# Performance work log

Measured on AMD Instinct MI355X. Metric: run time of the kernel, lower is better.

## Reference

```python
import jax, jax.numpy as jnp
import numpy as np

NH = 1024
NV = 31
LAYERS = 2
BS = 64
SEQ = 512
EPS = 1e-5


def _gru_layer(x_seq, h0, Wih, Whh, bih, bhh):
    """x_seq: [B,S,in], h0: [B,nh]. PyTorch GRU gate math. Returns [B,S,nh], h_last."""
    # Precompute input-side gates for all timesteps: [B,S,3nh]
    xg = jnp.einsum('bsi,gi->bsg', x_seq, Wih) + bih
    xg = jnp.swapaxes(xg, 0, 1)  # [S,B,3nh] for scan over time

    def step(h, xg_t):
        hg = h @ Whh.T + bhh  # [B,3nh]
        xr, xz, xn = jnp.split(xg_t, 3, axis=-1)
        hr, hz, hn = jnp.split(hg, 3, axis=-1)
        r = jax.nn.sigmoid(xr + hr)
        z = jax.nn.sigmoid(xz + hz)
        n = jnp.tanh(xn + r * hn)
        h_new = (1.0 - z) * n + z * h
        return h_new, h_new

    h_last, ys = jax.lax.scan(step, h0, xg)
    return jnp.swapaxes(ys, 0, 1), h_last  # [B,S,nh]


def setup_inputs() -> dict:
    key = jax.random.key(0)
    ks = jax.random.split(key, 16)
    s = 0.02
    inp = {
        'x': jax.random.randint(ks[0], (BS, SEQ), 0, NV),
        'h0': jnp.zeros((LAYERS, BS, NH), jnp.float32),
        'emb': jax.random.normal(ks[1], (NV, NH), jnp.float32) * s,
        'Wih0': jax.random.normal(ks[2], (3 * NH, NH), jnp.float32) * s,
        'Whh0': jax.random.normal(ks[3], (3 * NH, NH), jnp.float32) * s,
        'bih0': jnp.zeros((3 * NH,), jnp.float32),
        'bhh0': jnp.zeros((3 * NH,), jnp.float32),
        'Wih1': jax.random.normal(ks[4], (3 * NH, NH), jnp.float32) * s,
        'Whh1': jax.random.normal(ks[5], (3 * NH, NH), jnp.float32) * s,
        'bih1': jnp.zeros((3 * NH,), jnp.float32),
        'bhh1': jnp.zeros((3 * NH,), jnp.float32),
        'gamma': jnp.ones((NH,), jnp.float32),
        'beta': jnp.zeros((NH,), jnp.float32),
        'Wout': jax.random.normal(ks[6], (NV, NH), jnp.float32) * s,
        'bout': jnp.zeros((NV,), jnp.float32),
    }
    return inp


def reference(x, h0, emb, Wih0, Whh0, bih0, bhh0, Wih1, Whh1, bih1, bhh1,
              gamma, beta, Wout, bout):
    e = emb[x]  # [B,S,nh] embedding lookup
    y0, _ = _gru_layer(e, h0[0], Wih0, Whh0, bih0, bhh0)
    y1, _ = _gru_layer(y0, h0[1], Wih1, Whh1, bih1, bhh1)
    # BatchNorm1dFlat: flatten (B*S, nh), batch-statistics BN, reshape back
    flat = y1.reshape(-1, NH)
    mu = flat.mean(axis=0)
    var = flat.var(axis=0)  # biased, as in BN training
    bn = (y1 - mu) * jax.lax.rsqrt(var + EPS) * gamma + beta
    return bn @ Wout.T + bout  # [B,S,nv]
```

## Files before the change

kernel.cpp:

```cpp
#include <hip/hip_runtime.h>
#include <cstddef>
#include <stdint.h>

#define NHID 1024
#define NVOC 31
#define NB   64
#define NSEQ 512
#define NWRK 192
#define NGRID 256
#define NTHR 512
#define EPSV 1e-5f
#define RS   68
#define RS2  36
#define SL   (NB*NHID)
#define XG_SLOTS 16

typedef __attribute__((ext_vector_type(8))) short short8;
typedef __attribute__((ext_vector_type(4))) float float4v;

#define OFF_F0  0
#define OFF_F1  4096
#define OFF_F2  8192
#define OFF_FIN 12288
#define CNT_BYTES 12352

#define M_OFF_Y0  12544
#define M_OFF_Y1  (M_OFF_Y0 + 513ull*SL*2)
#define M_OFF_H1I (M_OFF_Y1 + 512ull*SL*2)
#define M_OFF_T0  (M_OFF_H1I + (unsigned long long)SL*2)
#define M_OFF_ST  (M_OFF_T0 + 31ull*3*NHID*4)
#define M_OFF_XG  (M_OFF_ST + 16384ull)

#define LDS_BYTES 65024

__device__ __forceinline__ unsigned short f2bf(float f){
  unsigned u = __builtin_bit_cast(unsigned, f);
  u += 0x7fffu + ((u >> 16) & 1u);
  return (unsigned short)(u >> 16);
}
__device__ __forceinline__ float bf2f(unsigned short h){
  unsigned u = ((unsigned)h) << 16;
  return __builtin_bit_cast(float, u);
}
__device__ __forceinline__ float sigm(float x){ return 1.f/(1.f + __expf(-x)); }
__device__ __forceinline__ float tanh_f(float x){ return 1.f - 2.f/(__expf(2.f*x) + 1.f); }

__device__ __forceinline__ void burn(float& d){
#pragma unroll
  for (int i=0;i<16;++i)
    asm volatile("v_fmac_f32 %0, %1, %2" : "+v"(d) : "v"(d), "v"(d));
}

__device__ __forceinline__ void setflag(unsigned* f, unsigned v){
  __hip_atomic_store(f, v, __ATOMIC_RELAXED, __HIP_MEMORY_SCOPE_AGENT);
}
__device__ __forceinline__ void waitflags64(const unsigned* f, int target, int lane, float& d){
  const unsigned* p = f + (size_t)lane*16;
  for(;;){
    int v = (int)__hip_atomic_load(p, __ATOMIC_RELAXED, __HIP_MEMORY_SCOPE_AGENT);
    if (__all(v >= target)) break;
    burn(d);
  }
  asm volatile("" ::: "memory");
}
__device__ __forceinline__ void waitflags32(const unsigned* f, int base32, int target, int lane, float& d){
  const unsigned* p = f + (size_t)(base32 + (lane & 31))*16;
  for(;;){
    int v = (int)__hip_atomic_load(p, __ATOMIC_RELAXED, __HIP_MEMORY_SCOPE_AGENT);
    if (__all(v >= target)) break;
    burn(d);
  }
  asm volatile("" ::: "memory");
}
__device__ __forceinline__ void waitflags2(const unsigned* f, int base2, int target, int lane, float& d){
  const unsigned* p = f + (size_t)(base2 + (lane & 1))*16;
  for(;;){
    int v = (int)__hip_atomic_load(p, __ATOMIC_RELAXED, __HIP_MEMORY_SCOPE_AGENT);
    if (__all(v >= target)) break;
    burn(d);
  }
  asm volatile("" ::: "memory");
}
__device__ __forceinline__ void waitflags_slow64(const unsigned* f, int target, int lane, float& d){
  const unsigned* p = f + (size_t)lane*16;
  for(;;){
    int v = (int)__hip_atomic_load(p, __ATOMIC_RELAXED, __HIP_MEMORY_SCOPE_AGENT);
    if (__all(v >= target)) break;
    burn(d); burn(d); burn(d); burn(d);
  }
  asm volatile("" ::: "memory");
}
__device__ __forceinline__ void sig(unsigned* c){
  __hip_atomic_fetch_add(c, 1u, __ATOMIC_RELAXED, __HIP_MEMORY_SCOPE_AGENT);
}
__device__ __forceinline__ void waitc(unsigned* c, unsigned v, float& d){
  while (__hip_atomic_load(c, __ATOMIC_RELAXED, __HIP_MEMORY_SCOPE_AGENT) < v)
    burn(d);
}

__device__ __forceinline__ void stc16(void* p, short8 v){
  asm volatile("global_store_dwordx4 %0, %1, off sc1"
               :: "v"((unsigned long long)(uintptr_t)p), "v"(v) : "memory");
}
__device__ __forceinline__ void stc4(void* p, float v){
  asm volatile("global_store_dword %0, %1, off sc1"
               :: "v"((unsigned long long)(uintptr_t)p), "v"(v) : "memory");
}
__device__ __forceinline__ void drain_vm(){
  asm volatile("s_waitcnt vmcnt(0)" ::: "memory");
}

__device__ __forceinline__ void load_a16_plain(const unsigned short* base, short8 (&f)[4][4]){
#pragma unroll
  for (int r=0;r<4;++r){
    const short8* p = (const short8*)(base + (size_t)r*16*NHID);
#pragma unroll
    for (int kt=0;kt<4;++kt) f[r][kt] = p[kt*4];
  }
}
__device__ __forceinline__ void gemm_frags(const short8 (&f)[4][4],
                                           const short8 (&bfr)[3][4],
                                           float* red, int lane, int wid)
{
  const int l15 = lane & 15, q = lane >> 4;
  float4v acc[4][3];
#pragma unroll
  for (int mt=0; mt<4; ++mt)
#pragma unroll
    for (int nt=0; nt<3; ++nt) acc[mt][nt] = (float4v){0.f,0.f,0.f,0.f};
#pragma unroll
  for (int kt=0; kt<4; ++kt){
#pragma unroll
    for (int nt=0; nt<3; ++nt){
      acc[0][nt] = __builtin_amdgcn_mfma_f32_16x16x32_bf16(f[0][kt], bfr[nt][kt], acc[0][nt],0,0,0);
      acc[1][nt] = __builtin_amdgcn_mfma_f32_16x16x32_bf16(f[1][kt], bfr[nt][kt], acc[1][nt],0,0,0);
      acc[2][nt] = __builtin_amdgcn_mfma_f32_16x16x32_bf16(f[2][kt], bfr[nt][kt], acc[2][nt],0,0,0);
      acc[3][nt] = __builtin_amdgcn_mfma_f32_16x16x32_bf16(f[3][kt], bfr[nt][kt], acc[3][nt],0,0,0);
    }
  }
  if (wid >= 4){
#pragma unroll
    for (int mt=0; mt<4; ++mt)
#pragma unroll
      for (int nt=0; nt<3; ++nt){
        int n = nt*16 + l15, row = mt*16 + q*4;
        *(float4v*)(red + ((wid-4)*48 + n)*RS + row) = acc[mt][nt];
      }
  }
  __syncthreads();
  if (wid < 4){
#pragma unroll
    for (int mt=0; mt<4; ++mt)
#pragma unroll
      for (int nt=0; nt<3; ++nt){
        int n = nt*16 + l15, row = mt*16 + q*4;
        float4v* p = (float4v*)(red + (wid*48 + n)*RS + row);
        float4v v = *p;
        *p = v + acc[mt][nt];
      }
  }
  __syncthreads();
}
__device__ __forceinline__ void load_bfrags(const float* W, const int* rowbase,
                                            short8 (&bfr)[3][4], int lane, int wid)
{
  const int l15 = lane & 15, q = lane >> 4;
#pragma unroll
  for (int nt=0; nt<3; ++nt){
    const float* wp0 = W + (size_t)(rowbase[nt] + l15)*NHID + wid*128 + q*8;
#pragma unroll
    for (int kt=0; kt<4; ++kt){
      const float* wp = wp0 + kt*32;
      short8 fr;
#pragma unroll
      for (int j=0;j<8;++j) fr[j] = (short)f2bf(wp[j]);
      bfr[nt][kt] = fr;
    }
  }
}

__device__ __forceinline__ void load_bfrags6(const float* W, int ch0,
                                             short8 (&bfr)[6][4], int lane, int wid)
{
  const int l15 = lane & 15, q = lane >> 4;
#pragma unroll
  for (int nt=0; nt<6; ++nt){
    int grow = (nt>>1)*NHID + ch0 + (nt&1)*16 + l15;
    const float* wp0 = W + (size_t)grow*NHID + wid*128 + q*8;
#pragma unroll
    for (int kt=0; kt<4; ++kt){
      const float* wp = wp0 + kt*32;
      short8 fr;
#pragma unroll
      for (int j=0;j<8;++j) fr[j] = (short)f2bf(wp[j]);
      bfr[nt][kt] = fr;
    }
  }
}
__device__ __forceinline__ void load_a2(const unsigned short* slab, int b0,
                                        short8 (&f)[2][4], int lane, int wid)
{
#pragma unroll
  for (int mt=0;mt<2;++mt){
    const short8* p = (const short8*)(slab + (size_t)(b0 + mt*16 + (lane&15))*NHID
                                      + wid*128 + (lane>>4)*8);
#pragma unroll
    for (int kt=0;kt<4;++kt) f[mt][kt] = p[kt*4];
  }
}
__device__ __forceinline__ void gemm2d(const short8 (&fA)[2][4],
                                       const short8 (&bfr)[6][4],
                                       float* red, int lane, int wid)
{
  const int l15 = lane & 15, q = lane >> 4;
  float4v acc[2][6];
#pragma unroll
  for (int mt=0; mt<2; ++mt)
#pragma unroll
    for (int nt=0; nt<6; ++nt) acc[mt][nt] = (float4v){0.f,0.f,0.f,0.f};
#pragma unroll
  for (int kt=0; kt<4; ++kt){
#pragma unroll
    for (int nt=0; nt<6; ++nt){
      acc[0][nt] = __builtin_amdgcn_mfma_f32_16x16x32_bf16(fA[0][kt], bfr[nt][kt], acc[0][nt],0,0,0);
      acc[1][nt] = __builtin_amdgcn_mfma_f32_16x16x32_bf16(fA[1][kt], bfr[nt][kt], acc[1][nt],0,0,0);
    }
  }
  if (wid >= 4){
#pragma unroll
    for (int mt=0; mt<2; ++mt)
#pragma unroll
      for (int nt=0; nt<6; ++nt){
        int n = nt*16 + l15, row = mt*16 + q*4;
        *(float4v*)(red + ((wid-4)*96 + n)*RS2 + row) = acc[mt][nt];
      }
  }
  __syncthreads();
  if (wid < 4){
#pragma unroll
    for (int mt=0; mt<2; ++mt)
#pragma unroll
      for (int nt=0; nt<6; ++nt){
        int n = nt*16 + l15, row = mt*16 + q*4;
        float4v* p = (float4v*)(red + (wid*96 + n)*RS2 + row);
        float4v v = *p;
        *p = v + acc[mt][nt];
      }
  }
  __syncthreads();
}

__global__ __launch_bounds__(NTHR, 2) void mgru_fused(
    const int*   __restrict__ x,    const float* __restrict__ h0,
    const float* __restrict__ emb,
    const float* __restrict__ Wih0, const float* __restrict__ Whh0,
    const float* __restrict__ bih0, const float* __restrict__ bhh0,
    const float* __restrict__ Wih1, const float* __restrict__ Whh1,
    const float* __restrict__ bih1, const float* __restrict__ bhh1,
    const float* __restrict__ gamma, const float* __restrict__ beta,
    const float* __restrict__ Wout, const float* __restrict__ bout,
    float* __restrict__ out, char* ws)
{
  __shared__ __align__(16) char smem[LDS_BYTES];
  float* red = (float*)smem;

  unsigned* f0  = (unsigned*)(ws + OFF_F0);
  unsigned* f1  = (unsigned*)(ws + OFF_F1);
  unsigned* f2  = (unsigned*)(ws + OFF_F2);
  unsigned* fin = (unsigned*)(ws + OFF_FIN);
  unsigned short* y0b   = (unsigned short*)(ws + M_OFF_Y0);
  unsigned short* y1    = (unsigned short*)(ws + M_OFF_Y1);
  unsigned short* h1i   = (unsigned short*)(ws + M_OFF_H1I);
  float*          T0    = (float*)(ws + M_OFF_T0);
  float*          stats = (float*)(ws + M_OFF_ST);
  float*          xgring= (float*)(ws + M_OFF_XG);

  const int tid  = threadIdx.x;
  const int lane = tid & 63;
  const int wid  = tid >> 6;
  const int wg   = blockIdx.x;
  const int l15 = lane & 15, q = lane >> 4;
  float dummy = (float)tid * 1e-30f + 1.0f;

  if (wg >= NWRK){
    for(;;){
      for (int i=0;i<64;++i) burn(dummy);
      unsigned v = __hip_atomic_load(fin, __ATOMIC_RELAXED, __HIP_MEMORY_SCOPE_AGENT);
      if (v >= (unsigned)NWRK) break;
    }
    if (tid == 0) __threadfence();
    __syncthreads();
    if (dummy == 1234.5678f) ((volatile float*)smem)[0] = dummy;
    goto epilogue;
  }

  {
    if (tid == 0) __threadfence();
    __syncthreads();

    const int role = (wg < 64) ? 0 : (wg < 128 ? 1 : 2);

    if (role == 0){
      const int rw = wg, bg = rw >> 5, cg = rw & 31;
      const int b0 = bg*32, ch0 = cg*32;
      const int fidx = bg*32 + cg;
      const int g = tid;
      const int b = b0 + (g & 31);
      const int oct = g >> 5;
      short8 bfr0[6][4];
      float hprev[8] = {0,0,0,0,0,0,0,0};
      float br[8], bz[8], bn[8];

      if (tid < 128){
        short8 pk;
#pragma unroll
        for (int j=0;j<8;++j){
          int ch = ch0 + oct*8 + j;
          hprev[j] = h0[(size_t)b*NHID + ch];
          br[j] = bhh0[ch]; bz[j] = bhh0[NHID + ch]; bn[j] = bhh0[2*NHID + ch];
          pk[j] = (short)f2bf(hprev[j]);
        }
        stc16(y0b + (size_t)b*NHID + ch0 + oct*8, pk);
        drain_vm();
      }
      __syncthreads();
      if (tid == 0) setflag(f0 + (size_t)fidx*16, 1u);

      for (int e = tid; e < NVOC*96; e += NTHR){
        int v = e / 96, n = e - v*96;
        int gate = n >> 5, c32 = n & 31;
        int grow = gate*NHID + ch0 + c32;
        const float4v* e4 = (const float4v*)(emb  + (size_t)v*NHID);
        const float4v* w4 = (const float4v*)(Wih0 + (size_t)grow*NHID);
        float acc = 0.f;
        for (int k=0;k<NHID/4;++k){
          float4v a = e4[k], bb = w4[k];
          acc += a[0]*bb[0] + a[1]*bb[1] + a[2]*bb[2] + a[3]*bb[3];
        }
        T0[(size_t)v*3*NHID + grow] = acc + bih0[grow];
      }
      load_bfrags6(Whh0, ch0, bfr0, lane, wid);
      __syncthreads();

      for (int t = 0; t < NSEQ; ++t){
        waitflags32(f0, bg*32, t+1, lane, dummy);
        short8 fA[2][4];
        load_a2(y0b + (size_t)t*SL, b0, fA, lane, wid);
        gemm2d(fA, bfr0, red, lane, wid);
        if (tid < 128){
          int tok = x[(size_t)b*NSEQ + t];
          const float* tp = T0 + (size_t)tok*3*NHID;
          int m = g & 31;
          short8 pk;
#pragma unroll
          for (int j=0;j<8;++j){
            int c32 = oct*8 + j, ch = ch0 + c32;
            float hr = br[j], hz = bz[j], hn = bn[j];
#pragma unroll
            for (int w=0;w<4;++w){
              hr += red[(w*96 +      c32)*RS2 + m];
              hz += red[(w*96 + 32 + c32)*RS2 + m];
              hn += red[(w*96 + 64 + c32)*RS2 + m];
            }
            float r = sigm(tp[ch] + hr);
            float z = sigm(tp[NHID + ch] + hz);
            float n = tanh_f(tp[2*NHID + ch] + r*hn);
            float hnv = (1.f - z)*n + z*hprev[j];
            hprev[j] = hnv;
            pk[j] = (short)f2bf(hnv);
          }
          stc16(y0b + (size_t)(t+1)*SL + (size_t)b*NHID + ch0 + oct*8, pk);
          drain_vm();
        }
        __syncthreads();
        if (tid == 0) setflag(f0 + (size_t)fidx*16, (unsigned)(t+2));
      }

    } else if (role == 1){
      const int sub = wg - 64, ch0 = sub*16;
      int rowbase[3] = {ch0, NHID + ch0, 2*NHID + ch0};
      short8 wf[3][4];
      load_bfrags(Wih1, rowbase, wf, lane, wid);
      __syncthreads();

      for (int t = 0; t < NSEQ; ++t){
        if ((t & 3) == 0 && t >= 16)
          waitflags_slow64(f2, t-11, lane, dummy);
        waitflags64(f0, t+2, lane, dummy);
        short8 fB[4][4];
        load_a16_plain(y0b + (size_t)(t+1)*SL + (size_t)l15*NHID + wid*128 + q*8, fB);
        gemm_frags(fB, wf, red, lane, wid);
        float* xgw = xgring + ((size_t)(t & (XG_SLOTS-1))*64 + (size_t)sub)*3072;
#pragma unroll
        for (int i=0;i<6;++i){
          int idx = tid + i*512;
          int n = idx >> 6, row = idx & 63;
          float v = bih1[(n>>4)*NHID + ch0 + (n&15)];
          v += red[(      n)*RS + row];
          v += red[( 48 + n)*RS + row];
          v += red[( 96 + n)*RS + row];
          v += red[(144 + n)*RS + row];
          stc4(xgw + idx, v);
        }
        drain_vm();
        __syncthreads();
        if (tid == 0) setflag(f1 + (size_t)sub*16, (unsigned)(t+2));
      }

    } else {
      const int rw = wg - 128, bg = rw >> 5, cg = rw & 31;
      const int b0 = bg*32, ch0 = cg*32;
      const int fidx = bg*32 + cg;
      const int g = tid;
      const int b = b0 + (g & 31);
      const int oct = g >> 5;
      short8 bfrH[6][4];
      float hprev[8] = {0,0,0,0,0,0,0,0};
      float bhr[8], bhz[8], bhn[8];
      float s1[8] = {0,0,0,0,0,0,0,0}, s2[8] = {0,0,0,0,0,0,0,0};

      if (tid < 128){
        short8 pk;
#pragma unroll
        for (int j=0;j<8;++j){
          int ch = ch0 + oct*8 + j;
          hprev[j] = h0[(size_t)NB*NHID + (size_t)b*NHID + ch];
          bhr[j] = bhh1[ch]; bhz[j] = bhh1[NHID + ch]; bhn[j] = bhh1[2*NHID + ch];
          pk[j] = (short)f2bf(hprev[j]);
        }
        stc16(h1i + (size_t)b*NHID + ch0 + oct*8, pk);
        drain_vm();
      }
      __syncthreads();
      if (tid == 0) setflag(f2 + (size_t)fidx*16, 1u);

      load_bfrags6(Whh1, ch0, bfrH, lane, wid);
      __syncthreads();

      for (int t = 0; t < NSEQ; ++t){
        waitflags32(f2, bg*32, t+1, lane, dummy);
        const unsigned short* hsrc = (t == 0) ? h1i : (y1 + (size_t)(t-1)*SL);
        short8 fH[2][4];
        load_a2(hsrc, b0, fH, lane, wid);
        gemm2d(fH, bfrH, red, lane, wid);
        float hrv[8], hzv[8], hnv_[8];
        if (tid < 128){
          int m = g & 31;
#pragma unroll
          for (int j=0;j<8;++j){
            int c32 = oct*8 + j;
            float hr = bhr[j], hz = bhz[j], hn = bhn[j];
#pragma unroll
            for (int w=0;w<4;++w){
              hr += red[(w*96 +      c32)*RS2 + m];
              hz += red[(w*96 + 32 + c32)*RS2 + m];
              hn += red[(w*96 + 64 + c32)*RS2 + m];
            }
            hrv[j] = hr; hzv[j] = hz; hnv_[j] = hn;
          }
        }
        waitflags2(f1, cg*2, t+2, lane, dummy);
        if (tid < 128){
          const float* xgp = xgring + (size_t)(t & (XG_SLOTS-1))*64*3072;
          short8 pk;
#pragma unroll
          for (int j=0;j<8;++j){
            int ch = ch0 + oct*8 + j;
            int sub1 = ch >> 4, c16 = ch & 15;
            const float* q0 = xgp + (size_t)sub1*3072 + (size_t)c16*64 + b;
            float xr = __hip_atomic_load(q0,           __ATOMIC_RELAXED, __HIP_MEMORY_SCOPE_AGENT);
            float xz = __hip_atomic_load(q0 + 16*64,   __ATOMIC_RELAXED, __HIP_MEMORY_SCOPE_AGENT);
            float xn = __hip_atomic_load(q0 + 32*64,   __ATOMIC_RELAXED, __HIP_MEMORY_SCOPE_AGENT);
            float r  = sigm(xr + hrv[j]);
            float z  = sigm(xz + hzv[j]);
            float nn = tanh_f(xn + r*hnv_[j]);
            float hnew = (1.f - z)*nn + z*hprev[j];
            hprev[j] = hnew;
            unsigned short hb = f2bf(hnew);
            pk[j] = (short)hb;
            float hq = bf2f(hb);
            s1[j] += hq; s2[j] += hq*hq;
          }
          stc16(y1 + (size_t)t*SL + (size_t)b*NHID + ch0 + oct*8, pk);
          drain_vm();
        }
        __syncthreads();
        if (tid == 0) setflag(f2 + (size_t)fidx*16, (unsigned)(t+2));
      }

      {
        float* sb = (float*)smem;
        __syncthreads();
        if (tid < 128){
#pragma unroll
          for (int j=0;j<8;++j) sb[(oct*8 + j)*32 + (g & 31)] = s1[j];
        }
        __syncthreads();
        if (tid < 32){
          float a = 0.f;
          for (int i=0;i<32;++i) a += sb[tid*32 + i];
          stats[(size_t)bg*2048 + ch0 + tid] = a;
        }
        __syncthreads();
        if (tid < 128){
#pragma unroll
          for (int j=0;j<8;++j) sb[(oct*8 + j)*32 + (g & 31)] = s2[j];
        }
        __syncthreads();
        if (tid < 32){
          float a = 0.f;
          for (int i=0;i<32;++i) a += sb[tid*32 + i];
          stats[(size_t)bg*2048 + 1024 + ch0 + tid] = a;
        }
      }
    }

    __syncthreads();
    if (tid == 0){
      __threadfence();
      sig(fin);
      waitc(fin, NWRK, dummy);
      __threadfence();
    }
    __syncthreads();
    if (dummy == 1234.5678f) ((volatile float*)smem)[0] = dummy;
  }

epilogue:
  {
    const float inv_n = 1.f/32768.f;

    float* bpart    = (float*)smem;
    float* bprime_l = (float*)(smem + 2048);
    {
      int v = tid >> 4, k0 = tid & 15;
      float partial = 0.f;
      if (v < NVOC){
        for (int k = k0; k < NHID; k += 16){
          float s1k = stats[k] + stats[2048 + k];
          float s2k = stats[1024 + k] + stats[3072 + k];
          float mu  = s1k*inv_n;
          float var = s2k*inv_n - mu*mu;
          float sc  = gamma[k]*rsqrtf(var + EPSV);
          partial += (beta[k] - mu*sc) * Wout[(size_t)v*NHID + k];
        }
      }
      bpart[tid] = partial;
    }
    __syncthreads();
    if (tid < 32){
      float bpv = 0.f;
      for (int j=0;j<16;++j) bpv += bpart[tid*16 + j];
      bprime_l[tid] = (tid < NVOC) ? (bpv + bout[tid]) : 0.f;
    }
    __syncthreads();
    float bp_a = bprime_l[l15];
    float bp_b = (l15 < 15) ? bprime_l[16 + l15] : 0.f;
    __syncthreads();

    unsigned short* wsc = (unsigned short*)smem;
    for (int e = tid; e < NVOC*1032; e += NTHR){
      int v = e / 1032, k = e - v*1032;
      float val = 0.f;
      if (k < NHID){
        float s1k = stats[k] + stats[2048 + k];
        float s2k = stats[1024 + k] + stats[3072 + k];
        float mu  = s1k*inv_n;
        float var = s2k*inv_n - mu*mu;
        float sc  = gamma[k]*rsqrtf(var + EPSV);
        val = Wout[(size_t)v*NHID + k] * sc;
      }
      wsc[e] = f2bf(val);
    }
    __syncthreads();

    int wglob = wg*8 + wid;
    if ((wglob & 3) == 0){
      int J = wglob >> 2;
      float4v acc[4][2];
#pragma unroll
      for (int mt=0;mt<4;++mt){ acc[mt][0] = (float4v){0,0,0,0}; acc[mt][1] = (float4v){0,0,0,0}; }
      const unsigned short* abase = y1 + (size_t)(J*64 + l15)*NHID + q*8;
      const short8 zero8 = (short8){0,0,0,0,0,0,0,0};
#pragma unroll 4
      for (int kt=0; kt<32; ++kt){
        short8 bv0 = *(const short8*)(wsc + (size_t)l15*1032 + kt*32 + q*8);
        short8 bv1 = (l15 < 15) ? *(const short8*)(wsc + (size_t)(16+l15)*1032 + kt*32 + q*8) : zero8;
        short8 a0 = *(const short8*)(abase + (size_t)kt*32);
        short8 a1 = *(const short8*)(abase + 16*NHID + (size_t)kt*32);
        short8 a2 = *(const short8*)(abase + 32*NHID + (size_t)kt*32);
        short8 a3 = *(const short8*)(abase + 48*NHID + (size_t)kt*32);
        acc[0][0] = __builtin_amdgcn_mfma_f32_16x16x32_bf16(a0, bv0, acc[0][0],0,0,0);
        acc[1][0] = __builtin_amdgcn_mfma_f32_16x16x32_bf16(a1, bv0, acc[1][0],0,0,0);
        acc[2][0] = __builtin_amdgcn_mfma_f32_16x16x32_bf16(a2, bv0, acc[2][0],0,0,0);
        acc[3][0] = __builtin_amdgcn_mfma_f32_16x16x32_bf16(a3, bv0, acc[3][0],0,0,0);
        acc[0][1] = __builtin_amdgcn_mfma_f32_16x16x32_bf16(a0, bv1, acc[0][1],0,0,0);
        acc[1][1] = __builtin_amdgcn_mfma_f32_16x16x32_bf16(a1, bv1, acc[1][1],0,0,0);
        acc[2][1] = __builtin_amdgcn_mfma_f32_16x16x32_bf16(a2, bv1, acc[2][1],0,0,0);
        acc[3][1] = __builtin_amdgcn_mfma_f32_16x16x32_bf16(a3, bv1, acc[3][1],0,0,0);
      }
#pragma unroll
      for (int mt=0;mt<4;++mt){
#pragma unroll
        for (int nt=0;nt<2;++nt){
          int v = nt*16 + l15;
          if (v < NVOC){
            float bpv = (nt==0) ? bp_a : bp_b;
            int r0 = J*64 + mt*16 + q*4;
#pragma unroll
            for (int i2=0;i2<4;++i2){
              int r = r0 + i2;
              int bb = r & 63, tt = r >> 6;
              out[(size_t)(bb*NSEQ + tt)*NVOC + v] = acc[mt][nt][i2] + bpv;
            }
          }
        }
      }
    }
  }
}

extern "C" void kernel_launch(void* const* d_in, const int* in_sizes, int n_in,
                              void* d_out, int out_size, void* d_ws, size_t ws_size,
                              hipStream_t stream) {
  (void)in_sizes; (void)n_in; (void)out_size; (void)ws_size;
  hipMemsetAsync(d_ws, 0, CNT_BYTES, stream);
  mgru_fused<<<dim3(NGRID), dim3(NTHR), 0, stream>>>(
      (const int*)d_in[0],  (const float*)d_in[1],  (const float*)d_in[2],
      (const float*)d_in[3], (const float*)d_in[4], (const float*)d_in[5],
      (const float*)d_in[6], (const float*)d_in[7], (const float*)d_in[8],
      (const float*)d_in[9], (const float*)d_in[10], (const float*)d_in[11],
      (const float*)d_in[12], (const float*)d_in[13], (const float*)d_in[14],
      (float*)d_out, (char*)d_ws);
}
```

Baseline: 4.171 ms.

## Retile layer-1 input-gate workers into 32-batch by 32-channel blocks with per-block flags

Layer-1 input-projection workgroups previously each covered 16 channels across all 64 batch rows and waited on all 64 layer-0 flags. They now each own a 32-batch by 32-channel tile, reuse the 2D GEMM helpers, and wait only on the 32 layer-0 flags of their batch group. Each consumer waits on a single matching producer flag and reads a contiguous xg tile. This narrows cross-workgroup dependencies so layer 1 can begin as soon as its batch half is ready. The cost is more weight fragments held in registers per workgroup.

```diff
diff --git a/kernel.cpp b/kernel.cpp
--- a/kernel.cpp
+++ b/kernel.cpp
@@ -10,7 +10,6 @@
 #define NGRID 256
 #define NTHR 512
 #define EPSV 1e-5f
-#define RS   68
 #define RS2  36
 #define SL   (NB*NHID)
 #define XG_SLOTS 16
@@ -54,15 +53,6 @@
 __device__ __forceinline__ void setflag(unsigned* f, unsigned v){
   __hip_atomic_store(f, v, __ATOMIC_RELAXED, __HIP_MEMORY_SCOPE_AGENT);
 }
-__device__ __forceinline__ void waitflags64(const unsigned* f, int target, int lane, float& d){
-  const unsigned* p = f + (size_t)lane*16;
-  for(;;){
-    int v = (int)__hip_atomic_load(p, __ATOMIC_RELAXED, __HIP_MEMORY_SCOPE_AGENT);
-    if (__all(v >= target)) break;
-    burn(d);
-  }
-  asm volatile("" ::: "memory");
-}
 __device__ __forceinline__ void waitflags32(const unsigned* f, int base32, int target, int lane, float& d){
   const unsigned* p = f + (size_t)(base32 + (lane & 31))*16;
   for(;;){
@@ -72,20 +62,15 @@
   }
   asm volatile("" ::: "memory");
 }
-__device__ __forceinline__ void waitflags2(const unsigned* f, int base2, int target, int lane, float& d){
-  const unsigned* p = f + (size_t)(base2 + (lane & 1))*16;
-  for(;;){
-    int v = (int)__hip_atomic_load(p, __ATOMIC_RELAXED, __HIP_MEMORY_SCOPE_AGENT);
-    if (__all(v >= target)) break;
+__device__ __forceinline__ void waitflag1(const unsigned* f, int idx, int target, float& d){
+  const unsigned* p = f + (size_t)idx*16;
+  while ((int)__hip_atomic_load(p, __ATOMIC_RELAXED, __HIP_MEMORY_SCOPE_AGENT) < target)
     burn(d);
-  }
   asm volatile("" ::: "memory");
 }
-__device__ __forceinline__ void waitflags_slow64(const unsigned* f, int target, int lane, float& d){
-  const unsigned* p = f + (size_t)lane*16;
-  for(;;){
-    int v = (int)__hip_atomic_load(p, __ATOMIC_RELAXED, __HIP_MEMORY_SCOPE_AGENT);
-    if (__all(v >= target)) break;
+__device__ __forceinline__ void waitflag1_slow(const unsigned* f, int idx, int target, float& d){
+  const unsigned* p = f + (size_t)idx*16;
+  while ((int)__hip_atomic_load(p, __ATOMIC_RELAXED, __HIP_MEMORY_SCOPE_AGENT) < target){
     burn(d); burn(d); burn(d); burn(d);
   }
   asm volatile("" ::: "memory");
@@ -108,75 +93,6 @@
 }
 __device__ __forceinline__ void drain_vm(){
   asm volatile("s_waitcnt vmcnt(0)" ::: "memory");
-}
-
-__device__ __forceinline__ void load_a16_plain(const unsigned short* base, short8 (&f)[4][4]){
-#pragma unroll
-  for (int r=0;r<4;++r){
-    const short8* p = (const short8*)(base + (size_t)r*16*NHID);
-#pragma unroll
-    for (int kt=0;kt<4;++kt) f[r][kt] = p[kt*4];
-  }
-}
-__device__ __forceinline__ void gemm_frags(const short8 (&f)[4][4],
-                                           const short8 (&bfr)[3][4],
-                                           float* red, int lane, int wid)
-{
-  const int l15 = lane & 15, q = lane >> 4;
-  float4v acc[4][3];
-#pragma unroll
-  for (int mt=0; mt<4; ++mt)
-#pragma unroll
-    for (int nt=0; nt<3; ++nt) acc[mt][nt] = (float4v){0.f,0.f,0.f,0.f};
-#pragma unroll
-  for (int kt=0; kt<4; ++kt){
-#pragma unroll
-    for (int nt=0; nt<3; ++nt){
-      acc[0][nt] = __builtin_amdgcn_mfma_f32_16x16x32_bf16(f[0][kt], bfr[nt][kt], acc[0][nt],0,0,0);
-      acc[1][nt] = __builtin_amdgcn_mfma_f32_16x16x32_bf16(f[1][kt], bfr[nt][kt], acc[1][nt],0,0,0);
-      acc[2][nt] = __builtin_amdgcn_mfma_f32_16x16x32_bf16(f[2][kt], bfr[nt][kt], acc[2][nt],0,0,0);
-      acc[3][nt] = __builtin_amdgcn_mfma_f32_16x16x32_bf16(f[3][kt], bfr[nt][kt], acc[3][nt],0,0,0);
-    }
-  }
-  if (wid >= 4){
-#pragma unroll
-    for (int mt=0; mt<4; ++mt)
-#pragma unroll
-      for (int nt=0; nt<3; ++nt){
-        int n = nt*16 + l15, row = mt*16 + q*4;
-        *(float4v*)(red + ((wid-4)*48 + n)*RS + row) = acc[mt][nt];
-      }
-  }
-  __syncthreads();
-  if (wid < 4){
-#pragma unroll
-    for (int mt=0; mt<4; ++mt)
-#pragma unroll
-      for (int nt=0; nt<3; ++nt){
-        int n = nt*16 + l15, row = mt*16 + q*4;
-        float4v* p = (float4v*)(red + (wid*48 + n)*RS + row);
-        float4v v = *p;
-        *p = v + acc[mt][nt];
-      }
-  }
-  __syncthreads();
-}
-__device__ __forceinline__ void load_bfrags(const float* W, const int* rowbase,
-                                            short8 (&bfr)[3][4], int lane, int wid)
-{
-  const int l15 = lane & 15, q = lane >> 4;
-#pragma unroll
-  for (int nt=0; nt<3; ++nt){
-    const float* wp0 = W + (size_t)(rowbase[nt] + l15)*NHID + wid*128 + q*8;
-#pragma unroll
-    for (int kt=0; kt<4; ++kt){
-      const float* wp = wp0 + kt*32;
-      short8 fr;
-#pragma unroll
-      for (int j=0;j<8;++j) fr[j] = (short)f2bf(wp[j]);
-      bfr[nt][kt] = fr;
-    }
-  }
 }
 
 __device__ __forceinline__ void load_bfrags6(const float* W, int ch0,
@@ -377,34 +293,35 @@
       }
 
     } else if (role == 1){
-      const int sub = wg - 64, ch0 = sub*16;
-      int rowbase[3] = {ch0, NHID + ch0, 2*NHID + ch0};
-      short8 wf[3][4];
-      load_bfrags(Wih1, rowbase, wf, lane, wid);
+      const int rw = wg - 64, bg = rw >> 5, cg = rw & 31;
+      const int b0 = bg*32, ch0 = cg*32;
+      const int fidx = bg*32 + cg;
+      short8 wf[6][4];
+      load_bfrags6(Wih1, ch0, wf, lane, wid);
       __syncthreads();
 
       for (int t = 0; t < NSEQ; ++t){
         if ((t & 3) == 0 && t >= 16)
-          waitflags_slow64(f2, t-11, lane, dummy);
-        waitflags64(f0, t+2, lane, dummy);
-        short8 fB[4][4];
-        load_a16_plain(y0b + (size_t)(t+1)*SL + (size_t)l15*NHID + wid*128 + q*8, fB);
-        gemm_frags(fB, wf, red, lane, wid);
-        float* xgw = xgring + ((size_t)(t & (XG_SLOTS-1))*64 + (size_t)sub)*3072;
+          waitflag1_slow(f2, fidx, t-11, dummy);
+        waitflags32(f0, bg*32, t+2, lane, dummy);
+        short8 fB[2][4];
+        load_a2(y0b + (size_t)(t+1)*SL, b0, fB, lane, wid);
+        gemm2d(fB, wf, red, lane, wid);
+        float* xgw = xgring + ((size_t)(t & (XG_SLOTS-1))*64 + (size_t)fidx)*3072;
 #pragma unroll
         for (int i=0;i<6;++i){
           int idx = tid + i*512;
-          int n = idx >> 6, row = idx & 63;
-          float v = bih1[(n>>4)*NHID + ch0 + (n&15)];
-          v += red[(      n)*RS + row];
-          v += red[( 48 + n)*RS + row];
-          v += red[( 96 + n)*RS + row];
-          v += red[(144 + n)*RS + row];
+          int n = idx >> 5, m = idx & 31;
+          float v = bih1[(n>>5)*NHID + ch0 + (n&31)];
+          v += red[(      n)*RS2 + m];
+          v += red[( 96 + n)*RS2 + m];
+          v += red[(192 + n)*RS2 + m];
+          v += red[(288 + n)*RS2 + m];
           stc4(xgw + idx, v);
         }
         drain_vm();
         __syncthreads();
-        if (tid == 0) setflag(f1 + (size_t)sub*16, (unsigned)(t+2));
+        if (tid == 0) setflag(f1 + (size_t)fidx*16, (unsigned)(t+2));
       }
 
     } else {
@@ -459,18 +376,17 @@
             hrv[j] = hr; hzv[j] = hz; hnv_[j] = hn;
           }
         }
-        waitflags2(f1, cg*2, t+2, lane, dummy);
+        waitflag1(f1, fidx, t+2, dummy);
         if (tid < 128){
-          const float* xgp = xgring + (size_t)(t & (XG_SLOTS-1))*64*3072;
+          const float* xgt = xgring + ((size_t)(t & (XG_SLOTS-1))*64 + (size_t)fidx)*3072;
+          int m = g & 31;
           short8 pk;
 #pragma unroll
           for (int j=0;j<8;++j){
-            int ch = ch0 + oct*8 + j;
-            int sub1 = ch >> 4, c16 = ch & 15;
-            const float* q0 = xgp + (size_t)sub1*3072 + (size_t)c16*64 + b;
-            float xr = __hip_atomic_load(q0,           __ATOMIC_RELAXED, __HIP_MEMORY_SCOPE_AGENT);
-            float xz = __hip_atomic_load(q0 + 16*64,   __ATOMIC_RELAXED, __HIP_MEMORY_SCOPE_AGENT);
-            float xn = __hip_atomic_load(q0 + 32*64,   __ATOMIC_RELAXED, __HIP_MEMORY_SCOPE_AGENT);
+            int c32 = oct*8 + j;
+            float xr = __hip_atomic_load(xgt + (size_t)(     c32)*32 + m, __ATOMIC_RELAXED, __HIP_MEMORY_SCOPE_AGENT);
+            float xz = __hip_atomic_load(xgt + (size_t)(32 + c32)*32 + m, __ATOMIC_RELAXED, __HIP_MEMORY_SCOPE_AGENT);
+            float xn = __hip_atomic_load(xgt + (size_t)(64 + c32)*32 + m, __ATOMIC_RELAXED, __HIP_MEMORY_SCOPE_AGENT);
             float r  = sigm(xr + hrv[j]);
             float z  = sigm(xz + hzv[j]);
             float nn = tanh_f(xn + r*hnv_[j]);
@@ -574,13 +490,14 @@
     }
     __syncthreads();
 
+    unsigned short* y1b = (unsigned short*)(ws + M_OFF_Y1);
     int wglob = wg*8 + wid;
     if ((wglob & 3) == 0){
       int J = wglob >> 2;
       float4v acc[4][2];
 #pragma unroll
       for (int mt=0;mt<4;++mt){ acc[mt][0] = (float4v){0,0,0,0}; acc[mt][1] = (float4v){0,0,0,0}; }
-      const unsigned short* abase = y1 + (size_t)(J*64 + l15)*NHID + q*8;
+      const unsigned short* abase = y1b + (size_t)(J*64 + l15)*NHID + q*8;
       const short8 zero8 = (short8){0,0,0,0,0,0,0,0};
 #pragma unroll 4
       for (int kt=0; kt<32; ++kt){
```

Measured after the change: 4.049 ms. 1.03x faster.
